# Kernel tuning notes

Measured on AMD Instinct MI355X. Metric: run time of the kernel, lower is better.

## Reference

```python
import jax, jax.numpy as jnp
import numpy as np
from jax.ops import segment_sum

N_NODES = 100000
N_EDGES = 3200000
N_GRAPHS = 64


def gcn_conv(x, W, b, src, dst, n_nodes):
    # Linear transform first (PyG GCNConv applies lin before propagate)
    h = x @ W  # [N, out]
    # Add self loops
    loop = jnp.arange(n_nodes, dtype=src.dtype)
    s = jnp.concatenate([src, loop])
    d = jnp.concatenate([dst, loop])
    # Symmetric normalization deg^-1/2 (deg counts incoming edges incl. self loop)
    deg = segment_sum(jnp.ones_like(d, dtype=h.dtype), d, num_segments=n_nodes)
    dinv = jnp.where(deg > 0, jax.lax.rsqrt(deg), 0.0)
    norm = dinv[s] * dinv[d]  # [E+N]
    # Gather messages from source, scale, scatter-add to target
    msg = h[s] * norm[:, None]
    out = segment_sum(msg, d, num_segments=n_nodes)
    return out + b


def setup_inputs() -> dict:
    key = jax.random.key(0)
    ks = jax.random.split(key, 6)
    x = jax.random.normal(ks[0], (N_NODES, 128), dtype=jnp.float32)
    edge_index = jax.random.randint(ks[1], (2, N_EDGES), 0, N_NODES, dtype=jnp.int64)
    batch = jnp.sort(jax.random.randint(ks[2], (N_NODES,), 0, N_GRAPHS, dtype=jnp.int64))
    W1 = jax.random.normal(ks[3], (128, 256), dtype=jnp.float32) * (1.0 / np.sqrt(128))
    b1 = jnp.zeros((256,), dtype=jnp.float32)
    W2 = jax.random.normal(ks[4], (256, 128), dtype=jnp.float32) * (1.0 / np.sqrt(256))
    b2 = jnp.zeros((128,), dtype=jnp.float32)
    return {"x": x, "edge_index": edge_index, "batch": batch,
            "W1": W1, "b1": b1, "W2": W2, "b2": b2, "num_graphs": N_GRAPHS}


def reference(x, edge_index, batch, W1, b1, W2, b2, num_graphs):
    n_nodes = x.shape[0]
    src, dst = edge_index[0], edge_index[1]
    # dropout(p=0.6, training=False) is identity at inference
    h = jax.nn.relu(gcn_conv(x, W1, b1, src, dst, n_nodes))
    h = gcn_conv(h, W2, b2, src, dst, n_nodes)
    # global_mean_pool by graph id
    sums = segment_sum(h, batch, num_segments=num_graphs)
    counts = segment_sum(jnp.ones((n_nodes,), dtype=h.dtype), batch, num_segments=num_graphs)
    return sums / jnp.maximum(counts, 1.0)[:, None]
```

## Files before the change

### kernel.cpp

```cpp
#include <hip/hip_runtime.h>
#include <hip/hip_bf16.h>
#include <stdint.h>

#define N_NODES 100000
#define N_EDGES 3200000
#define N_GRAPHS 64
#define BSH 8
#define NB 391
#define G_SC 512
#define EPB 6250

typedef unsigned int u32;
typedef unsigned short u16;
typedef __attribute__((ext_vector_type(8))) short bf16x8;
typedef __attribute__((ext_vector_type(4))) float f32x4;

__device__ __forceinline__ float bf_lo(u32 u){ return __uint_as_float(u << 16); }
__device__ __forceinline__ float bf_hi(u32 u){ return __uint_as_float(u & 0xffff0000u); }
__device__ __forceinline__ u16 f2bf(float f){
    union { __hip_bfloat16 h; u16 u; } c; c.h = __float2bfloat16(f); return c.u;
}
__device__ __forceinline__ u32 pack2(float a, float b){
    return (u32)f2bf(a) | ((u32)f2bf(b) << 16);
}

__global__ __launch_bounds__(512) void k_hist(const int* __restrict__ dst,
                                              int* __restrict__ hist){
    __shared__ int h[NB];
    int tid = threadIdx.x, g = blockIdx.x;
    for (int i = tid; i < NB; i += 512) h[i] = 0;
    __syncthreads();
    const int2* d2 = reinterpret_cast<const int2*>(dst + g * EPB);
    for (int i = tid; i < EPB / 2; i += 512){
        int2 d = d2[i];
        atomicAdd(&h[d.x >> BSH], 1);
        atomicAdd(&h[d.y >> BSH], 1);
    }
    __syncthreads();
    for (int i = tid; i < NB; i += 512) hist[i * G_SC + g] = h[i];
}

__global__ __launch_bounds__(512) void k_colscan(const int* __restrict__ hist,
                                                 int* __restrict__ cursors,
                                                 int* __restrict__ btot){
    __shared__ int sm[512];
    int b = blockIdx.x, tid = threadIdx.x;
    int v = hist[b * G_SC + tid];
    sm[tid] = v; __syncthreads();
    for (int off = 1; off < 512; off <<= 1){
        int t = (tid >= off) ? sm[tid - off] : 0;
        __syncthreads(); sm[tid] += t; __syncthreads();
    }
    cursors[b * G_SC + tid] = sm[tid] - v;
    if (tid == 511) btot[b] = sm[511];
}

__global__ __launch_bounds__(512) void k_bscan(const int* __restrict__ btot,
                                               int* __restrict__ bbase){
    __shared__ int sm[512];
    int tid = threadIdx.x;
    int v = (tid < NB) ? btot[tid] : 0;
    sm[tid] = v; __syncthreads();
    for (int off = 1; off < 512; off <<= 1){
        int t = (tid >= off) ? sm[tid - off] : 0;
        __syncthreads(); sm[tid] += t; __syncthreads();
    }
    if (tid < NB) bbase[tid] = sm[tid] - v;
    if (tid == 0) bbase[NB] = N_EDGES;
}

__global__ __launch_bounds__(512) void k_scatter(const int* __restrict__ src,
                                                 const int* __restrict__ dst,
                                                 const int* __restrict__ cursors,
                                                 const int* __restrict__ bbase,
                                                 uint2* __restrict__ pairs){
    __shared__ int cur[NB];
    int g = blockIdx.x, tid = threadIdx.x;
    for (int i = tid; i < NB; i += 512) cur[i] = cursors[i * G_SC + g] + bbase[i];
    __syncthreads();
    const int2* s2 = reinterpret_cast<const int2*>(src + g * EPB);
    const int2* d2 = reinterpret_cast<const int2*>(dst + g * EPB);
    for (int i = tid; i < EPB / 2; i += 512){
        int2 s = s2[i]; int2 d = d2[i];
        int p0 = atomicAdd(&cur[d.x >> BSH], 1);
        pairs[p0] = make_uint2((u32)s.x, (u32)d.x);
        int p1 = atomicAdd(&cur[d.y >> BSH], 1);
        pairs[p1] = make_uint2((u32)s.y, (u32)d.y);
    }
}

__global__ __launch_bounds__(512) void k_fine(const uint2* __restrict__ pairs,
                                              const int* __restrict__ bbase,
                                              int* __restrict__ offsets,
                                              float* __restrict__ dinv,
                                              int* __restrict__ csr_src){
    __shared__ int ldeg[256];
    __shared__ int ssc[256];
    __shared__ int lcur[256];
    int b = blockIdx.x, tid = threadIdx.x;
    int node0 = b << BSH;
    if (tid < 256) ldeg[tid] = 0;
    __syncthreads();
    int e0 = bbase[b], e1 = bbase[b + 1];
    for (int e = e0 + tid; e < e1; e += 512)
        atomicAdd(&ldeg[pairs[e].y - node0], 1);
    __syncthreads();
    int myDeg = (tid < 256) ? ldeg[tid] : 0;
    if (tid < 256) ssc[tid] = myDeg;
    __syncthreads();
    for (int off = 1; off < 256; off <<= 1){
        int t = 0;
        if (tid >= off && tid < 256) t = ssc[tid - off];
        __syncthreads();
        if (tid < 256) ssc[tid] += t;
        __syncthreads();
    }
    if (tid < 256){
        int excl = ssc[tid] - myDeg;
        int n = node0 + tid;
        if (n <= N_NODES) offsets[n] = e0 + excl;
        if (n < N_NODES)  dinv[n] = rsqrtf((float)myDeg + 1.0f);
        lcur[tid] = e0 + excl;
    }
    __syncthreads();
    for (int e = e0 + tid; e < e1; e += 512){
        uint2 p = pairs[e];
        int pos = atomicAdd(&lcur[p.y - node0], 1);
        csr_src[pos] = (int)p.x;
    }
}

__global__ void k_cvt_x(const float* __restrict__ x, const float* __restrict__ dinv,
                        u32* __restrict__ xb){
    int i = blockIdx.x * blockDim.x + threadIdx.x;
    if (i < N_NODES * 32){
        float w = dinv[i >> 5];
        float4 f = reinterpret_cast<const float4*>(x)[i];
        uint2 p = make_uint2(pack2(f.x * w, f.y * w), pack2(f.z * w, f.w * w));
        reinterpret_cast<uint2*>(xb)[i] = p;
    }
}

__global__ void k_cvt_w(const float* __restrict__ W1, const float* __restrict__ W2,
                        u16* __restrict__ w1t, u16* __restrict__ w2t){
    int i = blockIdx.x * blockDim.x + threadIdx.x;
    if (i < 128 * 256){
        int n = i / 128, k = i % 128;
        w1t[i] = f2bf(W1[k * 256 + n]);
    } else {
        int j = i - 128 * 256;
        int n = j / 256, k = j % 256;
        w2t[j] = f2bf(W2[k * 128 + n]);
    }
}

template<bool OUT_BF16>
__global__ __launch_bounds__(256) void k_agg(const u32* __restrict__ X,
                      const int* __restrict__ offs, const int* __restrict__ csr_src,
                      const float* __restrict__ dinv, void* __restrict__ out){
    int lane = threadIdx.x & 63;
    int v = blockIdx.x * 4 + (threadIdx.x >> 6);
    u32 u = X[v * 64 + lane];
    float a0 = bf_lo(u), a1 = bf_hi(u);
    int e1 = offs[v + 1];
    for (int e = offs[v]; e < e1; e += 64){
        int idx = e + lane;
        int sv = (idx < e1) ? csr_src[idx] : 0;
        int cnt = min(64, e1 - e);
        int j = 0;
        for (; j + 4 <= cnt; j += 4){
            int s0 = __shfl(sv, j), s1 = __shfl(sv, j+1), s2 = __shfl(sv, j+2), s3 = __shfl(sv, j+3);
            u32 u0 = X[s0*64 + lane], u1 = X[s1*64 + lane], u2 = X[s2*64 + lane], u3 = X[s3*64 + lane];
            a0 += (bf_lo(u0) + bf_lo(u1)) + (bf_lo(u2) + bf_lo(u3));
            a1 += (bf_hi(u0) + bf_hi(u1)) + (bf_hi(u2) + bf_hi(u3));
        }
        for (; j < cnt; j++){
            int s = __shfl(sv, j);
            u32 uu = X[s*64 + lane];
            a0 += bf_lo(uu); a1 += bf_hi(uu);
        }
    }
    float w = dinv[v];
    a0 *= w; a1 *= w;
    if (OUT_BF16){
        ((u32*)out)[v*64 + lane] = pack2(a0, a1);
    } else {
        ((float2*)out)[v*64 + lane] = make_float2(a0, a1);
    }
}

template<int BK, int BN, bool RELU, bool BIAS, bool SCALE>
__global__ __launch_bounds__(256) void k_gemm(const u16* __restrict__ A, const u16* __restrict__ BT,
                        const float* __restrict__ bias, const float* __restrict__ rowscale,
                        u16* __restrict__ C, int M){
    extern __shared__ char smem[];
    char* As = smem;
    char* Bs = smem + 64 * BK * 2;
    const int tid = threadIdx.x;
    const int rowbytes = BK * 2;
    {
        const int a16 = 64 * rowbytes / 16;
        for (int it = tid; it < a16; it += 256){
            int flat = it * 16;
            int r = flat / rowbytes, cb = flat % rowbytes;
            int grow = blockIdx.x * 64 + r;
            int4 val = make_int4(0,0,0,0);
            if (grow < M) val = *reinterpret_cast<const int4*>(A + grow * BK + cb / 2);
            *reinterpret_cast<int4*>(As + r * rowbytes + (cb ^ ((r & 7) << 4))) = val;
        }
        const int b16 = BN * rowbytes / 16;
        for (int it = tid; it < b16; it += 256){
            int flat = it * 16;
            int r = flat / rowbytes, cb = flat % rowbytes;
            int4 val = *reinterpret_cast<const int4*>(BT + r * BK + cb / 2);
            *reinterpret_cast<int4*>(Bs + r * rowbytes + (cb ^ ((r & 7) << 4))) = val;
        }
    }
    __syncthreads();

    const int wid = tid >> 6, lane = tid & 63;
    const int r0 = wid * 16;
    constexpr int NF = BN / 16;
    f32x4 acc[NF];
#pragma unroll
    for (int i = 0; i < NF; i++) acc[i] = (f32x4){0.f,0.f,0.f,0.f};
    const int ar = r0 + (lane & 15);
    const int koff = (lane >> 4) * 8;
#pragma unroll
    for (int kb = 0; kb < BK / 32; kb++){
        int kbyte = (kb * 32 + koff) * 2;
        bf16x8 aF = *reinterpret_cast<const bf16x8*>(As + ar * rowbytes + (kbyte ^ ((ar & 7) << 4)));
#pragma unroll
        for (int nf = 0; nf < NF; nf++){
            int bn = nf * 16 + (lane & 15);
            bf16x8 bF = *reinterpret_cast<const bf16x8*>(Bs + bn * rowbytes + (kbyte ^ ((bn & 7) << 4)));
            acc[nf] = __builtin_amdgcn_mfma_f32_16x16x32_bf16(aF, bF, acc[nf], 0, 0, 0);
        }
    }
#pragma unroll
    for (int nf = 0; nf < NF; nf++){
        int col = nf * 16 + (lane & 15);
        float bv = BIAS ? bias[col] : 0.f;
#pragma unroll
        for (int j = 0; j < 4; j++){
            int grow = blockIdx.x * 64 + r0 + (lane >> 4) * 4 + j;
            if (grow < M){
                float val = acc[nf][j] + bv;
                if (RELU) val = fmaxf(val, 0.f);
                if (SCALE) val *= rowscale[grow];
                C[grow * BN + col] = f2bf(val);
            }
        }
    }
}

__global__ void k_pool(const float* __restrict__ agg2f, const int* __restrict__ batch,
                       float* __restrict__ psum, float* __restrict__ counts){
    const int NPB = 200;
    int n0 = blockIdx.x * NPB, n1 = min(n0 + NPB, N_NODES);
    int tid = threadIdx.x;
    float racc = 0.f; int gcur = batch[n0]; int runlen = 0;
    for (int n = n0; n < n1; n++){
        int g = batch[n];
        if (g != gcur){
            atomicAdd(&psum[gcur * 128 + tid], racc);
            if (tid == 0) atomicAdd(&counts[gcur], (float)runlen);
            racc = 0.f; runlen = 0; gcur = g;
        }
        racc += agg2f[n * 128 + tid];
        runlen++;
    }
    atomicAdd(&psum[gcur * 128 + tid], racc);
    if (tid == 0) atomicAdd(&counts[gcur], (float)runlen);
}

__global__ void k_final(const float* __restrict__ psum, const float* __restrict__ counts,
                        const float* __restrict__ b2, float* __restrict__ out){
    int g = blockIdx.x, c = threadIdx.x;
    out[g * 128 + c] = psum[g * 128 + c] / fmaxf(counts[g], 1.0f) + b2[c];
}

extern "C" void kernel_launch(void* const* d_in, const int* in_sizes, int n_in,
                              void* d_out, int out_size, void* d_ws, size_t ws_size,
                              hipStream_t stream){
    const float* x   = (const float*)d_in[0];
    const int*   ei  = (const int*)d_in[1];
    const int* batch = (const int*)d_in[2];
    const float* W1  = (const float*)d_in[3];
    const float* b1  = (const float*)d_in[4];
    const float* W2  = (const float*)d_in[5];
    const float* b2  = (const float*)d_in[6];
    float* out = (float*)d_out;
    const int* esrc = ei;
    const int* edst = ei + N_EDGES;

    char* w = (char*)d_ws;
    size_t off = 0;
    auto alloc = [&](size_t bytes) -> char* {
        char* p = w + off; off += (bytes + 255) & ~size_t(255); return p;
    };
    float* dinv     = (float*)alloc((size_t)N_NODES * 4);
    int*   offsets  = (int*)  alloc((size_t)(N_NODES + 1) * 4);
    int*   hist     = (int*)  alloc((size_t)NB * G_SC * 4);
    int*   cursors  = (int*)  alloc((size_t)NB * G_SC * 4);
    int*   btot     = (int*)  alloc((size_t)NB * 4);
    int*   bbase    = (int*)  alloc((size_t)(NB + 1) * 4);
    int*   csr_src  = (int*)  alloc((size_t)N_EDGES * 4);
    u32*   xb       = (u32*)  alloc((size_t)N_NODES * 64 * 4);
    u16*   aggx     = (u16*)  alloc((size_t)N_NODES * 128 * 2);
    u16*   h        = (u16*)  alloc((size_t)N_NODES * 256 * 2);
    u16*   t        = (u16*)  alloc((size_t)N_NODES * 128 * 2);
    u16*   w1t      = (u16*)  alloc(128 * 256 * 2);
    u16*   w2t      = (u16*)  alloc(256 * 128 * 2);
    float* psum     = (float*)alloc((size_t)N_GRAPHS * 128 * 4);
    float* counts   = (float*)alloc((size_t)N_GRAPHS * 4);
    float* agg2f    = (float*)h;
    uint2* pairs    = (uint2*)h;

    hipMemsetAsync(psum, 0, (size_t)N_GRAPHS * 128 * 4, stream);
    hipMemsetAsync(counts, 0, (size_t)N_GRAPHS * 4, stream);

    k_hist   <<<G_SC, 512, 0, stream>>>(edst, hist);
    k_colscan<<<NB, 512, 0, stream>>>(hist, cursors, btot);
    k_bscan  <<<1, 512, 0, stream>>>(btot, bbase);
    k_scatter<<<G_SC, 512, 0, stream>>>(esrc, edst, cursors, bbase, pairs);
    k_fine   <<<NB, 512, 0, stream>>>(pairs, bbase, offsets, dinv, csr_src);

    k_cvt_x<<<12500, 256, 0, stream>>>(x, dinv, xb);
    k_cvt_w<<<256, 256, 0, stream>>>(W1, W2, w1t, w2t);

    k_agg<true><<<25000, 256, 0, stream>>>(xb, offsets, csr_src, dinv, aggx);

    hipFuncSetAttribute(reinterpret_cast<const void*>(&k_gemm<128, 256, true, true, false>),
                        hipFuncAttributeMaxDynamicSharedMemorySize, 64*128*2 + 256*128*2);
    hipFuncSetAttribute(reinterpret_cast<const void*>(&k_gemm<256, 128, false, false, true>),
                        hipFuncAttributeMaxDynamicSharedMemorySize, 64*256*2 + 128*256*2);

    k_gemm<128, 256, true, true, false><<<1563, 256, 64*128*2 + 256*128*2, stream>>>(
        aggx, w1t, b1, nullptr, h, N_NODES);
    k_gemm<256, 128, false, false, true><<<1563, 256, 64*256*2 + 128*256*2, stream>>>(
        h, w2t, nullptr, dinv, t, N_NODES);
    k_agg<false><<<25000, 256, 0, stream>>>((const u32*)t, offsets, csr_src, dinv, (void*)agg2f);
    k_pool <<<500, 128, 0, stream>>>(agg2f, batch, psum, counts);
    k_final<<<N_GRAPHS, 128, 0, stream>>>(psum, counts, b2, out);
}
```

Measured before the change: 619.1 us.

## Pack edge pairs into 32 bits, unroll gather by 8, read GEMM weights from global

The CSR build now packs the source index and the low 8 bits of the destination into one 32-bit word instead of a uint2, halving the pairs buffer traffic. The aggregation loop is unrolled to 8 outstanding gathers per iteration for more memory-level parallelism. The GEMM no longer stages the weight matrix in LDS and reads B fragments straight from global/L2, which cuts shared memory per block and may raise occupancy at the cost of repeated global reads. The pooling kernel uses smaller chunks with more blocks.

```diff
diff --git a/kernel.cpp b/kernel.cpp
--- a/kernel.cpp
+++ b/kernel.cpp
@@ -73,7 +73,7 @@
                                                  const int* __restrict__ dst,
                                                  const int* __restrict__ cursors,
                                                  const int* __restrict__ bbase,
-                                                 uint2* __restrict__ pairs){
+                                                 u32* __restrict__ pairs){
     __shared__ int cur[NB];
     int g = blockIdx.x, tid = threadIdx.x;
     for (int i = tid; i < NB; i += 512) cur[i] = cursors[i * G_SC + g] + bbase[i];
@@ -83,13 +83,13 @@
     for (int i = tid; i < EPB / 2; i += 512){
         int2 s = s2[i]; int2 d = d2[i];
         int p0 = atomicAdd(&cur[d.x >> BSH], 1);
-        pairs[p0] = make_uint2((u32)s.x, (u32)d.x);
+        pairs[p0] = (u32)s.x | ((u32)(d.x & 255) << 24);
         int p1 = atomicAdd(&cur[d.y >> BSH], 1);
-        pairs[p1] = make_uint2((u32)s.y, (u32)d.y);
-    }
-}
-
-__global__ __launch_bounds__(512) void k_fine(const uint2* __restrict__ pairs,
+        pairs[p1] = (u32)s.y | ((u32)(d.y & 255) << 24);
+    }
+}
+
+__global__ __launch_bounds__(512) void k_fine(const u32* __restrict__ pairs,
                                               const int* __restrict__ bbase,
                                               int* __restrict__ offsets,
                                               float* __restrict__ dinv,
@@ -103,7 +103,7 @@
     __syncthreads();
     int e0 = bbase[b], e1 = bbase[b + 1];
     for (int e = e0 + tid; e < e1; e += 512)
-        atomicAdd(&ldeg[pairs[e].y - node0], 1);
+        atomicAdd(&ldeg[pairs[e] >> 24], 1);
     __syncthreads();
     int myDeg = (tid < 256) ? ldeg[tid] : 0;
     if (tid < 256) ssc[tid] = myDeg;
@@ -124,9 +124,9 @@
     }
     __syncthreads();
     for (int e = e0 + tid; e < e1; e += 512){
-        uint2 p = pairs[e];
-        int pos = atomicAdd(&lcur[p.y - node0], 1);
-        csr_src[pos] = (int)p.x;
+        u32 p = pairs[e];
+        int pos = atomicAdd(&lcur[p >> 24], 1);
+        csr_src[pos] = (int)(p & 0xFFFFFFu);
     }
 }
 
@@ -168,11 +168,15 @@
         int sv = (idx < e1) ? csr_src[idx] : 0;
         int cnt = min(64, e1 - e);
         int j = 0;
-        for (; j + 4 <= cnt; j += 4){
-            int s0 = __shfl(sv, j), s1 = __shfl(sv, j+1), s2 = __shfl(sv, j+2), s3 = __shfl(sv, j+3);
+        for (; j + 8 <= cnt; j += 8){
+            int s0 = __shfl(sv, j),   s1 = __shfl(sv, j+1), s2 = __shfl(sv, j+2), s3 = __shfl(sv, j+3);
+            int s4 = __shfl(sv, j+4), s5 = __shfl(sv, j+5), s6 = __shfl(sv, j+6), s7 = __shfl(sv, j+7);
             u32 u0 = X[s0*64 + lane], u1 = X[s1*64 + lane], u2 = X[s2*64 + lane], u3 = X[s3*64 + lane];
-            a0 += (bf_lo(u0) + bf_lo(u1)) + (bf_lo(u2) + bf_lo(u3));
-            a1 += (bf_hi(u0) + bf_hi(u1)) + (bf_hi(u2) + bf_hi(u3));
+            u32 u4 = X[s4*64 + lane], u5 = X[s5*64 + lane], u6 = X[s6*64 + lane], u7 = X[s7*64 + lane];
+            a0 += (bf_lo(u0) + bf_lo(u1)) + (bf_lo(u2) + bf_lo(u3))
+                + (bf_lo(u4) + bf_lo(u5)) + (bf_lo(u6) + bf_lo(u7));
+            a1 += (bf_hi(u0) + bf_hi(u1)) + (bf_hi(u2) + bf_hi(u3))
+                + (bf_hi(u4) + bf_hi(u5)) + (bf_hi(u6) + bf_hi(u7));
         }
         for (; j < cnt; j++){
             int s = __shfl(sv, j);
@@ -193,28 +197,17 @@
 __global__ __launch_bounds__(256) void k_gemm(const u16* __restrict__ A, const u16* __restrict__ BT,
                         const float* __restrict__ bias, const float* __restrict__ rowscale,
                         u16* __restrict__ C, int M){
-    extern __shared__ char smem[];
-    char* As = smem;
-    char* Bs = smem + 64 * BK * 2;
+    __shared__ char As[64 * BK * 2];
     const int tid = threadIdx.x;
     const int rowbytes = BK * 2;
-    {
-        const int a16 = 64 * rowbytes / 16;
-        for (int it = tid; it < a16; it += 256){
-            int flat = it * 16;
-            int r = flat / rowbytes, cb = flat % rowbytes;
-            int grow = blockIdx.x * 64 + r;
-            int4 val = make_int4(0,0,0,0);
-            if (grow < M) val = *reinterpret_cast<const int4*>(A + grow * BK + cb / 2);
-            *reinterpret_cast<int4*>(As + r * rowbytes + (cb ^ ((r & 7) << 4))) = val;
-        }
-        const int b16 = BN * rowbytes / 16;
-        for (int it = tid; it < b16; it += 256){
-            int flat = it * 16;
-            int r = flat / rowbytes, cb = flat % rowbytes;
-            int4 val = *reinterpret_cast<const int4*>(BT + r * BK + cb / 2);
-            *reinterpret_cast<int4*>(Bs + r * rowbytes + (cb ^ ((r & 7) << 4))) = val;
-        }
+    const int units = 8 * BK;
+    for (int it = tid; it < units; it += 256){
+        int flat = it * 16;
+        int r = flat / rowbytes, cb = flat % rowbytes;
+        int grow = blockIdx.x * 64 + r;
+        int4 val = make_int4(0,0,0,0);
+        if (grow < M) val = *reinterpret_cast<const int4*>(A + (size_t)grow * BK + cb / 2);
+        *reinterpret_cast<int4*>(As + r * rowbytes + (cb ^ ((r & 7) << 4))) = val;
     }
     __syncthreads();
 
@@ -233,7 +226,7 @@
 #pragma unroll
         for (int nf = 0; nf < NF; nf++){
             int bn = nf * 16 + (lane & 15);
-            bf16x8 bF = *reinterpret_cast<const bf16x8*>(Bs + bn * rowbytes + (kbyte ^ ((bn & 7) << 4)));
+            bf16x8 bF = *reinterpret_cast<const bf16x8*>(BT + bn * BK + kb * 32 + koff);
             acc[nf] = __builtin_amdgcn_mfma_f32_16x16x32_bf16(aF, bF, acc[nf], 0, 0, 0);
         }
     }
@@ -248,7 +241,7 @@
                 float val = acc[nf][j] + bv;
                 if (RELU) val = fmaxf(val, 0.f);
                 if (SCALE) val *= rowscale[grow];
-                C[grow * BN + col] = f2bf(val);
+                C[(size_t)grow * BN + col] = f2bf(val);
             }
         }
     }
@@ -256,7 +249,7 @@
 
 __global__ void k_pool(const float* __restrict__ agg2f, const int* __restrict__ batch,
                        float* __restrict__ psum, float* __restrict__ counts){
-    const int NPB = 200;
+    const int NPB = 100;
     int n0 = blockIdx.x * NPB, n1 = min(n0 + NPB, N_NODES);
     int tid = threadIdx.x;
     float racc = 0.f; int gcur = batch[n0]; int runlen = 0;
@@ -267,7 +260,7 @@
             if (tid == 0) atomicAdd(&counts[gcur], (float)runlen);
             racc = 0.f; runlen = 0; gcur = g;
         }
-        racc += agg2f[n * 128 + tid];
+        racc += agg2f[(size_t)n * 128 + tid];
         runlen++;
     }
     atomicAdd(&psum[gcur * 128 + tid], racc);
@@ -315,7 +308,7 @@
     float* psum     = (float*)alloc((size_t)N_GRAPHS * 128 * 4);
     float* counts   = (float*)alloc((size_t)N_GRAPHS * 4);
     float* agg2f    = (float*)h;
-    uint2* pairs    = (uint2*)h;
+    u32*   pairs    = (u32*)h;
 
     hipMemsetAsync(psum, 0, (size_t)N_GRAPHS * 128 * 4, stream);
     hipMemsetAsync(counts, 0, (size_t)N_GRAPHS * 4, stream);
@@ -330,17 +323,11 @@
     k_cvt_w<<<256, 256, 0, stream>>>(W1, W2, w1t, w2t);
 
     k_agg<true><<<25000, 256, 0, stream>>>(xb, offsets, csr_src, dinv, aggx);
-
-    hipFuncSetAttribute(reinterpret_cast<const void*>(&k_gemm<128, 256, true, true, false>),
-                        hipFuncAttributeMaxDynamicSharedMemorySize, 64*128*2 + 256*128*2);
-    hipFuncSetAttribute(reinterpret_cast<const void*>(&k_gemm<256, 128, false, false, true>),
-                        hipFuncAttributeMaxDynamicSharedMemorySize, 64*256*2 + 128*256*2);
-
-    k_gemm<128, 256, true, true, false><<<1563, 256, 64*128*2 + 256*128*2, stream>>>(
+    k_gemm<128, 256, true, true, false><<<1563, 256, 0, stream>>>(
         aggx, w1t, b1, nullptr, h, N_NODES);
-    k_gemm<256, 128, false, false, true><<<1563, 256, 64*256*2 + 128*256*2, stream>>>(
+    k_gemm<256, 128, false, false, true><<<1563, 256, 0, stream>>>(
         h, w2t, nullptr, dinv, t, N_NODES);
     k_agg<false><<<25000, 256, 0, stream>>>((const u32*)t, offsets, csr_src, dinv, (void*)agg2f);
-    k_pool <<<500, 128, 0, stream>>>(agg2f, batch, psum, counts);
+    k_pool <<<1000, 128, 0, stream>>>(agg2f, batch, psum, counts);
     k_final<<<N_GRAPHS, 128, 0, stream>>>(psum, counts, b2, out);
 }
```

Result: faster. 596.0 us (-3.7%).
